# Kernel optimization log

Measured on AMD Instinct MI355X. Metric: run time of the kernel, lower is better.

## Reference

```python
import jax, jax.numpy as jnp
import numpy as np

USER_NUM = 50000
ITEM_NUM = 50000
N = USER_NUM + ITEM_NUM
VT_DIM = 512
CAT_NUM = 1000
CAT_DIM = 32
HIDDEN = 128
OUT = 64
E = 2_000_000
BAG = 5


def setup_inputs() -> dict:
    key = jax.random.key(0)
    ks = jax.random.split(key, 12)
    inp = {
        "vt_feature": jax.random.normal(ks[0], (ITEM_NUM, VT_DIM), jnp.float32),
        "cat_indices": jax.random.randint(ks[1], (ITEM_NUM * BAG,), 0, CAT_NUM),
        "cat_offsets": jnp.arange(ITEM_NUM) * BAG,
        "edge_index": jax.random.randint(ks[2], (2, E), 0, N),
        # learned parameters
        "cat_table": jax.random.normal(ks[3], (CAT_NUM, CAT_DIM), jnp.float32) * 0.1,
        "fuse_w": jax.random.normal(ks[4], (HIDDEN, VT_DIM + CAT_DIM), jnp.float32) * (1.0 / np.sqrt(VT_DIM + CAT_DIM)),
        "user": jax.random.normal(ks[5], (USER_NUM, HIDDEN), jnp.float32) * 0.1,
        "w1_l": jax.random.normal(ks[6], (HIDDEN, HIDDEN), jnp.float32) * (1.0 / np.sqrt(HIDDEN)),
        "b1": jnp.zeros((HIDDEN,), jnp.float32),
        "w1_r": jax.random.normal(ks[7], (HIDDEN, HIDDEN), jnp.float32) * (1.0 / np.sqrt(HIDDEN)),
        "w2_l": jax.random.normal(ks[8], (OUT, HIDDEN), jnp.float32) * (1.0 / np.sqrt(HIDDEN)),
        "b2": jnp.zeros((OUT,), jnp.float32),
        "w2_r": jax.random.normal(ks[9], (OUT, HIDDEN), jnp.float32) * (1.0 / np.sqrt(HIDDEN)),
    }
    return inp


def _embedding_bag_mean(table, indices, offsets, num_bags):
    # EmbeddingBag(mode='mean') with offsets: segment-mean of table lookups.
    pos = jnp.arange(indices.shape[0])
    seg = jnp.searchsorted(offsets, pos, side="right") - 1  # bag id per index
    sums = jax.ops.segment_sum(table[indices], seg, num_segments=num_bags)
    cnt = jax.ops.segment_sum(jnp.ones_like(pos, jnp.float32), seg, num_segments=num_bags)
    return sums / jnp.maximum(cnt, 1.0)[:, None]


def _sage_conv(x, edge_index, w_l, b_l, w_r):
    # PyG SAGEConv (aggr='mean'): lin_l(mean_{j->i} x_j) + lin_r(x_i)
    src, dst = edge_index[0], edge_index[1]
    agg = jax.ops.segment_sum(x[src], dst, num_segments=N)
    deg = jax.ops.segment_sum(jnp.ones((src.shape[0],), x.dtype), dst, num_segments=N)
    agg = agg / jnp.maximum(deg, 1.0)[:, None]
    return agg @ w_l.T + b_l + x @ w_r.T


def reference(vt_feature, cat_indices, cat_offsets, edge_index, cat_table,
              fuse_w, user, w1_l, b1, w1_r, w2_l, b2, w2_r):
    cat_emb = _embedding_bag_mean(cat_table, cat_indices, cat_offsets, ITEM_NUM)
    item_feat = jnp.concatenate([vt_feature, cat_emb], axis=1) @ fuse_w.T
    x0 = jnp.concatenate([user, item_feat], axis=0)  # [N, hidden]
    x1 = jax.nn.leaky_relu(_sage_conv(x0, edge_index, w1_l, b1, w1_r), negative_slope=0.01)
    # dropout is identity in eval mode
    x2 = _sage_conv(x1, edge_index, w2_l, b2, w2_r)
    return x2
```

## Files before the change

### kernel.cpp

```cpp
#include <hip/hip_runtime.h>

#define USER_N   50000
#define ITEM_N   50000
#define NNODE    100000
#define VT_DIM   512
#define CAT_DIM  32
#define HIDDEN   128
#define OUTD     64
#define PADCAP   64

typedef __attribute__((ext_vector_type(8))) short short8;
typedef __attribute__((ext_vector_type(4))) float f32x4;

__device__ __forceinline__ float bf2f(unsigned short u) {
    return __uint_as_float(((unsigned int)u) << 16);
}
__device__ __forceinline__ unsigned short f2bf(float f) {
    unsigned int u = __float_as_uint(f);
    unsigned int r = u + 0x7fffu + ((u >> 16) & 1u);
    return (unsigned short)(r >> 16);
}

__global__ __launch_bounds__(256) void k_catemb(const float* __restrict__ cat_table,
                                                const int* __restrict__ cat_idx,
                                                const int* __restrict__ cat_off,
                                                unsigned short* __restrict__ catemb,
                                                int item_num, int total_idx) {
    int gid = blockIdx.x * 256 + threadIdx.x;
    int item = gid >> 5;
    int d = gid & 31;
    if (item >= item_num) return;
    int s = cat_off[item];
    int e = (item + 1 < item_num) ? cat_off[item + 1] : total_idx;
    float acc = 0.f;
    for (int j = s; j < e; ++j) {
        int idx = cat_idx[j];
        acc += cat_table[idx * CAT_DIM + d];
    }
    int cnt = e - s;
    float inv = 1.f / (float)(cnt > 0 ? cnt : 1);
    catemb[(size_t)item * CAT_DIM + d] = f2bf(acc * inv);
}

__global__ __launch_bounds__(256) void k_copy_user(const float* __restrict__ user,
                                                   unsigned short* __restrict__ x0, int n4) {
    int gid = blockIdx.x * 256 + threadIdx.x;
    if (gid >= n4) return;
    float4 v = ((const float4*)user)[gid];
    ushort4 o;
    o.x = f2bf(v.x); o.y = f2bf(v.y); o.z = f2bf(v.z); o.w = f2bf(v.w);
    ((ushort4*)x0)[gid] = o;
}

#define ASTR 40

__global__ __launch_bounds__(256, 2) void k_fuse_mfma(const float* __restrict__ vt,
                                                      const unsigned short* __restrict__ catemb,
                                                      const float* __restrict__ fw,
                                                      unsigned short* __restrict__ x0) {
    __shared__ __align__(16) unsigned short Al[256 * ASTR];
    __shared__ __align__(16) unsigned short Bl[128 * ASTR];
    int tid = threadIdx.x;
    int wave = tid >> 6, lane = tid & 63, quad = lane >> 4, l16 = lane & 15;
    int br0 = blockIdx.x * 256;
    int arow = br0 + tid;

    f32x4 acc[4][8];
#pragma unroll
    for (int m = 0; m < 4; m++)
#pragma unroll
        for (int n = 0; n < 8; n++) acc[m][n] = (f32x4){0.f, 0.f, 0.f, 0.f};

    for (int kb = 0; kb < 17; ++kb) {
        if (kb < 16) {
            if (arow < ITEM_N) {
                const float* src = vt + (size_t)arow * VT_DIM + kb * 32;
#pragma unroll
                for (int i = 0; i < 8; i++) {
                    float4 v = ((const float4*)src)[i];
                    ushort4 o;
                    o.x = f2bf(v.x); o.y = f2bf(v.y); o.z = f2bf(v.z); o.w = f2bf(v.w);
                    *(ushort4*)&Al[tid * ASTR + i * 4] = o;
                }
            } else {
                ushort4 z = {0, 0, 0, 0};
#pragma unroll
                for (int i = 0; i < 8; i++) *(ushort4*)&Al[tid * ASTR + i * 4] = z;
            }
        } else {
            if (arow < ITEM_N) {
                const uint4* src = (const uint4*)(catemb + (size_t)arow * CAT_DIM);
                *(uint4*)&Al[tid * ASTR]      = src[0];
                *(uint4*)&Al[tid * ASTR + 8]  = src[1];
                *(uint4*)&Al[tid * ASTR + 16] = src[2];
                *(uint4*)&Al[tid * ASTR + 24] = src[3];
            } else {
                uint4 z = {0, 0, 0, 0};
                *(uint4*)&Al[tid * ASTR]      = z;
                *(uint4*)&Al[tid * ASTR + 8]  = z;
                *(uint4*)&Al[tid * ASTR + 16] = z;
                *(uint4*)&Al[tid * ASTR + 24] = z;
            }
        }
        {
            int n = tid & 127, kh = tid >> 7;
            const float* src = fw + (size_t)n * (VT_DIM + CAT_DIM) + kb * 32 + kh * 16;
#pragma unroll
            for (int i = 0; i < 4; i++) {
                float4 v = ((const float4*)src)[i];
                ushort4 o;
                o.x = f2bf(v.x); o.y = f2bf(v.y); o.z = f2bf(v.z); o.w = f2bf(v.w);
                *(ushort4*)&Bl[n * ASTR + kh * 16 + i * 4] = o;
            }
        }
        __syncthreads();
        short8 av[4];
#pragma unroll
        for (int m = 0; m < 4; m++)
            av[m] = *(const short8*)&Al[(wave * 64 + m * 16 + l16) * ASTR + quad * 8];
#pragma unroll
        for (int nf = 0; nf < 8; nf++) {
            short8 bv = *(const short8*)&Bl[(nf * 16 + l16) * ASTR + quad * 8];
#pragma unroll
            for (int m = 0; m < 4; m++)
                acc[m][nf] = __builtin_amdgcn_mfma_f32_16x16x32_bf16(av[m], bv, acc[m][nf], 0, 0, 0);
        }
        __syncthreads();
    }
    int rbase = br0 + wave * 64;
#pragma unroll
    for (int m = 0; m < 4; m++) {
#pragma unroll
        for (int r = 0; r < 4; r++) {
            int row = rbase + m * 16 + quad * 4 + r;
            if (row < ITEM_N) {
#pragma unroll
                for (int nf = 0; nf < 8; nf++) {
                    int col = nf * 16 + l16;
                    x0[(size_t)(USER_N + row) * HIDDEN + col] = f2bf(acc[m][nf][r]);
                }
            }
        }
    }
}

__global__ __launch_bounds__(256, 2) void k_l1_mfma(const unsigned short* __restrict__ agg1,
                                                    const unsigned short* __restrict__ x0,
                                                    const float* __restrict__ w1l,
                                                    const float* __restrict__ w1r,
                                                    const float* __restrict__ b1,
                                                    unsigned short* __restrict__ x1) {
    __shared__ __align__(16) unsigned short Al[256 * ASTR];
    __shared__ __align__(16) unsigned short Bl[128 * ASTR];
    int tid = threadIdx.x;
    int wave = tid >> 6, lane = tid & 63, quad = lane >> 4, l16 = lane & 15;
    int br0 = blockIdx.x * 256;
    int arow = br0 + tid;

    f32x4 acc[4][8];
#pragma unroll
    for (int m = 0; m < 4; m++)
#pragma unroll
        for (int n = 0; n < 8; n++) acc[m][n] = (f32x4){0.f, 0.f, 0.f, 0.f};

    for (int kb = 0; kb < 8; ++kb) {
        const unsigned short* abase = (kb < 4) ? agg1 : x0;
        int kc = (kb & 3) * 32;
        if (arow < NNODE) {
            const uint4* src = (const uint4*)(abase + (size_t)arow * HIDDEN + kc);
            *(uint4*)&Al[tid * ASTR]      = src[0];
            *(uint4*)&Al[tid * ASTR + 8]  = src[1];
            *(uint4*)&Al[tid * ASTR + 16] = src[2];
            *(uint4*)&Al[tid * ASTR + 24] = src[3];
        } else {
            uint4 z = {0, 0, 0, 0};
            *(uint4*)&Al[tid * ASTR]      = z;
            *(uint4*)&Al[tid * ASTR + 8]  = z;
            *(uint4*)&Al[tid * ASTR + 16] = z;
            *(uint4*)&Al[tid * ASTR + 24] = z;
        }
        {
            int n = tid & 127, kh = tid >> 7;
            const float* src = ((kb < 4) ? w1l : w1r) + (size_t)n * HIDDEN + kc + kh * 16;
#pragma unroll
            for (int i = 0; i < 4; i++) {
                float4 v = ((const float4*)src)[i];
                ushort4 o;
                o.x = f2bf(v.x); o.y = f2bf(v.y); o.z = f2bf(v.z); o.w = f2bf(v.w);
                *(ushort4*)&Bl[n * ASTR + kh * 16 + i * 4] = o;
            }
        }
        __syncthreads();
        short8 av[4];
#pragma unroll
        for (int m = 0; m < 4; m++)
            av[m] = *(const short8*)&Al[(wave * 64 + m * 16 + l16) * ASTR + quad * 8];
#pragma unroll
        for (int nf = 0; nf < 8; nf++) {
            short8 bv = *(const short8*)&Bl[(nf * 16 + l16) * ASTR + quad * 8];
#pragma unroll
            for (int m = 0; m < 4; m++)
                acc[m][nf] = __builtin_amdgcn_mfma_f32_16x16x32_bf16(av[m], bv, acc[m][nf], 0, 0, 0);
        }
        __syncthreads();
    }
    float bias[8];
#pragma unroll
    for (int nf = 0; nf < 8; nf++) bias[nf] = b1[nf * 16 + l16];
    int rbase = br0 + wave * 64;
#pragma unroll
    for (int m = 0; m < 4; m++) {
#pragma unroll
        for (int r = 0; r < 4; r++) {
            int row = rbase + m * 16 + quad * 4 + r;
            if (row < NNODE) {
#pragma unroll
                for (int nf = 0; nf < 8; nf++) {
                    int col = nf * 16 + l16;
                    float v = acc[m][nf][r] + bias[nf];
                    v = (v >= 0.f) ? v : 0.01f * v;
                    x1[(size_t)row * HIDDEN + col] = f2bf(v);
                }
            }
        }
    }
}

__global__ __launch_bounds__(256, 2) void k_l2_mfma(const unsigned short* __restrict__ x1,
                                                    const float* __restrict__ w2l,
                                                    const float* __restrict__ w2r,
                                                    const float* __restrict__ b2,
                                                    unsigned short* __restrict__ y1,
                                                    float* __restrict__ outw) {
    __shared__ __align__(16) unsigned short Al[256 * ASTR];
    __shared__ __align__(16) unsigned short Bl[128 * ASTR];
    int tid = threadIdx.x;
    int wave = tid >> 6, lane = tid & 63, quad = lane >> 4, l16 = lane & 15;
    int br0 = blockIdx.x * 256;
    int arow = br0 + tid;

    f32x4 acc[4][8];
#pragma unroll
    for (int m = 0; m < 4; m++)
#pragma unroll
        for (int n = 0; n < 8; n++) acc[m][n] = (f32x4){0.f, 0.f, 0.f, 0.f};

    for (int kb = 0; kb < 4; ++kb) {
        int kc = kb * 32;
        if (arow < NNODE) {
            const uint4* src = (const uint4*)(x1 + (size_t)arow * HIDDEN + kc);
            *(uint4*)&Al[tid * ASTR]      = src[0];
            *(uint4*)&Al[tid * ASTR + 8]  = src[1];
            *(uint4*)&Al[tid * ASTR + 16] = src[2];
            *(uint4*)&Al[tid * ASTR + 24] = src[3];
        } else {
            uint4 z = {0, 0, 0, 0};
            *(uint4*)&Al[tid * ASTR]      = z;
            *(uint4*)&Al[tid * ASTR + 8]  = z;
            *(uint4*)&Al[tid * ASTR + 16] = z;
            *(uint4*)&Al[tid * ASTR + 24] = z;
        }
        {
            int n = tid & 127, kh = tid >> 7;
            const float* wsrc = (n < 64) ? (w2l + (size_t)n * HIDDEN)
                                         : (w2r + (size_t)(n - 64) * HIDDEN);
            const float* src = wsrc + kc + kh * 16;
#pragma unroll
            for (int i = 0; i < 4; i++) {
                float4 v = ((const float4*)src)[i];
                ushort4 o;
                o.x = f2bf(v.x); o.y = f2bf(v.y); o.z = f2bf(v.z); o.w = f2bf(v.w);
                *(ushort4*)&Bl[n * ASTR + kh * 16 + i * 4] = o;
            }
        }
        __syncthreads();
        short8 av[4];
#pragma unroll
        for (int m = 0; m < 4; m++)
            av[m] = *(const short8*)&Al[(wave * 64 + m * 16 + l16) * ASTR + quad * 8];
#pragma unroll
        for (int nf = 0; nf < 8; nf++) {
            short8 bv = *(const short8*)&Bl[(nf * 16 + l16) * ASTR + quad * 8];
#pragma unroll
            for (int m = 0; m < 4; m++)
                acc[m][nf] = __builtin_amdgcn_mfma_f32_16x16x32_bf16(av[m], bv, acc[m][nf], 0, 0, 0);
        }
        __syncthreads();
    }
    float bias2[4];
#pragma unroll
    for (int nf = 0; nf < 4; nf++) bias2[nf] = b2[nf * 16 + l16];
    int rbase = br0 + wave * 64;
#pragma unroll
    for (int m = 0; m < 4; m++) {
#pragma unroll
        for (int r = 0; r < 4; r++) {
            int row = rbase + m * 16 + quad * 4 + r;
            if (row < NNODE) {
#pragma unroll
                for (int nf = 0; nf < 4; nf++) {
                    int col = nf * 16 + l16;
                    y1[(size_t)row * OUTD + col] = f2bf(acc[m][nf][r]);
                }
#pragma unroll
                for (int nf = 4; nf < 8; nf++) {
                    int col = (nf - 4) * 16 + l16;
                    outw[(size_t)row * OUTD + col] = acc[m][nf][r] + bias2[nf - 4];
                }
            }
        }
    }
}

__global__ __launch_bounds__(256) void k_deg(const int* __restrict__ dst, int ne4, int ne, int* __restrict__ deg) {
    int t = blockIdx.x * 256 + threadIdx.x;
    int base = t * 4;
    if (t < ne4) {
        int4 d4 = *(const int4*)&dst[base];
        atomicAdd(&deg[d4.x], 1);
        atomicAdd(&deg[d4.y], 1);
        atomicAdd(&deg[d4.z], 1);
        atomicAdd(&deg[d4.w], 1);
    } else {
        for (int e = base; e < ne; ++e) atomicAdd(&deg[dst[e]], 1);
    }
}

__global__ __launch_bounds__(256) void k_scanA(const int* __restrict__ deg, int n, int* __restrict__ bsum) {
    __shared__ int sd[256];
    int i = blockIdx.x * 256 + threadIdx.x;
    sd[threadIdx.x] = (i < n) ? deg[i] : 0;
    __syncthreads();
    for (int o = 128; o > 0; o >>= 1) {
        if (threadIdx.x < o) sd[threadIdx.x] += sd[threadIdx.x + o];
        __syncthreads();
    }
    if (threadIdx.x == 0) bsum[blockIdx.x] = sd[0];
}

__global__ __launch_bounds__(512) void k_scanB(const int* __restrict__ bsum, int nb, int* __restrict__ boff) {
    __shared__ int sd[512];
    int t = threadIdx.x;
    int v = (t < nb) ? bsum[t] : 0;
    sd[t] = v;
    __syncthreads();
    for (int o = 1; o < 512; o <<= 1) {
        int x = 0;
        if (t >= o) x = sd[t - o];
        __syncthreads();
        sd[t] += x;
        __syncthreads();
    }
    if (t < nb) boff[t] = sd[t] - v;
}

__global__ __launch_bounds__(256) void k_scanC(const int* __restrict__ deg, int n,
                                               const int* __restrict__ boff,
                                               int* __restrict__ offs, int* __restrict__ cursor, int ne) {
    __shared__ int sd[256];
    int i = blockIdx.x * 256 + threadIdx.x;
    int v = (i < n) ? deg[i] : 0;
    sd[threadIdx.x] = v;
    __syncthreads();
    for (int o = 1; o < 256; o <<= 1) {
        int x = 0;
        if (threadIdx.x >= o) x = sd[threadIdx.x - o];
        __syncthreads();
        sd[threadIdx.x] += x;
        __syncthreads();
    }
    if (i < n) {
        int ex = boff[blockIdx.x] + sd[threadIdx.x] - v;
        offs[i] = ex;
        cursor[i] = ex;
    }
    if (i == 0) offs[n] = ne;
}

__global__ __launch_bounds__(256) void k_scatter(const int* __restrict__ src, const int* __restrict__ dst,
                                                 int ne4, int ne, int* __restrict__ cursor, int* __restrict__ csr) {
    int t = blockIdx.x * 256 + threadIdx.x;
    int base = t * 4;
    if (t < ne4) {
        int4 d4 = *(const int4*)&dst[base];
        int4 s4 = *(const int4*)&src[base];
        int p0 = atomicAdd(&cursor[d4.x], 1);
        int p1 = atomicAdd(&cursor[d4.y], 1);
        int p2 = atomicAdd(&cursor[d4.z], 1);
        int p3 = atomicAdd(&cursor[d4.w], 1);
        csr[p0] = s4.x;
        csr[p1] = s4.y;
        csr[p2] = s4.z;
        csr[p3] = s4.w;
    } else {
        for (int e = base; e < ne; ++e) {
            int slot = atomicAdd(&cursor[dst[e]], 1);
            csr[slot] = src[e];
        }
    }
}

__global__ __launch_bounds__(256) void k_scatter_pad(const int* __restrict__ src, const int* __restrict__ dst,
                                                     int ne4, int ne, int* __restrict__ cursor,
                                                     int* __restrict__ csrp) {
    int t = blockIdx.x * 256 + threadIdx.x;
    int base = t * 4;
    if (t < ne4) {
        int4 d4 = *(const int4*)&dst[base];
        int4 s4 = *(const int4*)&src[base];
        int p0 = atomicAdd(&cursor[d4.x], 1);
        int p1 = atomicAdd(&cursor[d4.y], 1);
        int p2 = atomicAdd(&cursor[d4.z], 1);
        int p3 = atomicAdd(&cursor[d4.w], 1);
        if (p0 < PADCAP) csrp[d4.x * PADCAP + p0] = s4.x;
        if (p1 < PADCAP) csrp[d4.y * PADCAP + p1] = s4.y;
        if (p2 < PADCAP) csrp[d4.z * PADCAP + p2] = s4.z;
        if (p3 < PADCAP) csrp[d4.w * PADCAP + p3] = s4.w;
    } else {
        for (int e = base; e < ne; ++e) {
            int d = dst[e];
            int slot = atomicAdd(&cursor[d], 1);
            if (slot < PADCAP) csrp[d * PADCAP + slot] = src[e];
        }
    }
}

__global__ __launch_bounds__(256) void k_agg1(const unsigned short* __restrict__ x0,
                                              const int* __restrict__ offs,
                                              const int* __restrict__ cnts,
                                              int pad,
                                              const int* __restrict__ csr,
                                              unsigned short* __restrict__ agg1) {
    int wid = (blockIdx.x << 2) + (threadIdx.x >> 6);
    if (wid >= NNODE) return;
    int lane = threadIdx.x & 63;
    int half = lane >> 5;
    int l32 = lane & 31;
    int s, e, d;
    if (pad) {
        s = wid << 6;
        int c = cnts[wid];
        d = c;
        e = s + (c < PADCAP ? c : PADCAP);
    } else {
        s = offs[wid];
        e = offs[wid + 1];
        d = e - s;
    }
    float a0 = 0.f, a1 = 0.f, a2 = 0.f, a3 = 0.f;
    int j = s;
    for (; j + 16 <= e; j += 16) {
        int sn[8];
#pragma unroll
        for (int u = 0; u < 8; u++) sn[u] = csr[j + 2 * u + half];
        ushort4 v[8];
#pragma unroll
        for (int u = 0; u < 8; u++) v[u] = *(const ushort4*)&x0[(size_t)sn[u] * HIDDEN + l32 * 4];
#pragma unroll
        for (int u = 0; u < 8; u++) {
            a0 += bf2f(v[u].x);
            a1 += bf2f(v[u].y);
            a2 += bf2f(v[u].z);
            a3 += bf2f(v[u].w);
        }
    }
    for (; j + 8 <= e; j += 8) {
        int sn0 = csr[j     + half];
        int sn1 = csr[j + 2 + half];
        int sn2 = csr[j + 4 + half];
        int sn3 = csr[j + 6 + half];
        ushort4 v0 = *(const ushort4*)&x0[(size_t)sn0 * HIDDEN + l32 * 4];
        ushort4 v1 = *(const ushort4*)&x0[(size_t)sn1 * HIDDEN + l32 * 4];
        ushort4 v2 = *(const ushort4*)&x0[(size_t)sn2 * HIDDEN + l32 * 4];
        ushort4 v3 = *(const ushort4*)&x0[(size_t)sn3 * HIDDEN + l32 * 4];
        a0 += bf2f(v0.x) + bf2f(v1.x) + bf2f(v2.x) + bf2f(v3.x);
        a1 += bf2f(v0.y) + bf2f(v1.y) + bf2f(v2.y) + bf2f(v3.y);
        a2 += bf2f(v0.z) + bf2f(v1.z) + bf2f(v2.z) + bf2f(v3.z);
        a3 += bf2f(v0.w) + bf2f(v1.w) + bf2f(v2.w) + bf2f(v3.w);
    }
    for (; j < e; j += 2) {
        int myj = j + half;
        bool ok = (myj < e);
        int sn = ok ? csr[myj] : csr[j];
        float w = ok ? 1.f : 0.f;
        ushort4 v = *(const ushort4*)&x0[(size_t)sn * HIDDEN + l32 * 4];
        a0 += w * bf2f(v.x);
        a1 += w * bf2f(v.y);
        a2 += w * bf2f(v.z);
        a3 += w * bf2f(v.w);
    }
    a0 += __shfl_xor(a0, 32, 64);
    a1 += __shfl_xor(a1, 32, 64);
    a2 += __shfl_xor(a2, 32, 64);
    a3 += __shfl_xor(a3, 32, 64);
    float inv = 1.f / (float)(d > 0 ? d : 1);
    if (half == 0) {
        ushort4 o;
        o.x = f2bf(a0 * inv);
        o.y = f2bf(a1 * inv);
        o.z = f2bf(a2 * inv);
        o.w = f2bf(a3 * inv);
        *(ushort4*)&agg1[(size_t)wid * HIDDEN + l32 * 4] = o;
    }
}

__global__ __launch_bounds__(256) void k_agg2_out(const unsigned short* __restrict__ y1,
                                                  const int* __restrict__ offs,
                                                  const int* __restrict__ cnts,
                                                  int pad,
                                                  const int* __restrict__ csr,
                                                  float* __restrict__ out) {
    int wid = (blockIdx.x << 2) + (threadIdx.x >> 6);
    if (wid >= NNODE) return;
    int lane = threadIdx.x & 63;
    int quad = lane >> 4;
    int l16 = lane & 15;
    int s, e, d;
    if (pad) {
        s = wid << 6;
        int c = cnts[wid];
        d = c;
        e = s + (c < PADCAP ? c : PADCAP);
    } else {
        s = offs[wid];
        e = offs[wid + 1];
        d = e - s;
    }
    float a0 = 0.f, a1 = 0.f, a2 = 0.f, a3 = 0.f;
    int j = s;
    for (; j + 16 <= e; j += 16) {
        int sn0 = csr[j      + quad];
        int sn1 = csr[j + 4  + quad];
        int sn2 = csr[j + 8  + quad];
        int sn3 = csr[j + 12 + quad];
        ushort4 v0 = *(const ushort4*)&y1[(size_t)sn0 * OUTD + l16 * 4];
        ushort4 v1 = *(const ushort4*)&y1[(size_t)sn1 * OUTD + l16 * 4];
        ushort4 v2 = *(const ushort4*)&y1[(size_t)sn2 * OUTD + l16 * 4];
        ushort4 v3 = *(const ushort4*)&y1[(size_t)sn3 * OUTD + l16 * 4];
        a0 += bf2f(v0.x) + bf2f(v1.x) + bf2f(v2.x) + bf2f(v3.x);
        a1 += bf2f(v0.y) + bf2f(v1.y) + bf2f(v2.y) + bf2f(v3.y);
        a2 += bf2f(v0.z) + bf2f(v1.z) + bf2f(v2.z) + bf2f(v3.z);
        a3 += bf2f(v0.w) + bf2f(v1.w) + bf2f(v2.w) + bf2f(v3.w);
    }
    for (; j < e; j += 4) {
        int myj = j + quad;
        bool ok = (myj < e);
        int sn = ok ? csr[myj] : csr[j];
        float w = ok ? 1.f : 0.f;
        ushort4 v = *(const ushort4*)&y1[(size_t)sn * OUTD + l16 * 4];
        a0 += w * bf2f(v.x);
        a1 += w * bf2f(v.y);
        a2 += w * bf2f(v.z);
        a3 += w * bf2f(v.w);
    }
    a0 += __shfl_xor(a0, 16, 64);
    a1 += __shfl_xor(a1, 16, 64);
    a2 += __shfl_xor(a2, 16, 64);
    a3 += __shfl_xor(a3, 16, 64);
    a0 += __shfl_xor(a0, 32, 64);
    a1 += __shfl_xor(a1, 32, 64);
    a2 += __shfl_xor(a2, 32, 64);
    a3 += __shfl_xor(a3, 32, 64);
    float inv = 1.f / (float)(d > 0 ? d : 1);
    if (quad == 0) {
        float4* op = (float4*)&out[(size_t)wid * OUTD + l16 * 4];
        float4 prev = *op;
        float4 o;
        o.x = a0 * inv + prev.x;
        o.y = a1 * inv + prev.y;
        o.z = a2 * inv + prev.z;
        o.w = a3 * inv + prev.w;
        *op = o;
    }
}

extern "C" void kernel_launch(void* const* d_in, const int* in_sizes, int n_in,
                              void* d_out, int out_size, void* d_ws, size_t ws_size,
                              hipStream_t stream) {
    const float* vt      = (const float*)d_in[0];
    const int*   cat_idx = (const int*)d_in[1];
    const int*   cat_off = (const int*)d_in[2];
    const int*   ei      = (const int*)d_in[3];
    const float* cat_tab = (const float*)d_in[4];
    const float* fuse_w  = (const float*)d_in[5];
    const float* user    = (const float*)d_in[6];
    const float* w1l     = (const float*)d_in[7];
    const float* b1      = (const float*)d_in[8];
    const float* w1r     = (const float*)d_in[9];
    const float* w2l     = (const float*)d_in[10];
    const float* b2      = (const float*)d_in[11];
    const float* w2r     = (const float*)d_in[12];
    float* out = (float*)d_out;

    const int ne = in_sizes[3] / 2;
    const int ne4 = ne / 4;
    const int total_idx = in_sizes[1];
    const int* esrc = ei;
    const int* edst = ei + ne;

    const size_t SZ_X0  = (size_t)NNODE * HIDDEN * 2;
    const size_t SZ_PAD = (size_t)NNODE * PADCAP * 4;
    const size_t SZ_CSR = (size_t)ne * 4;
    const size_t SZ_INT = (size_t)NNODE * 4;

    size_t need_pad = SZ_X0 * 3 + SZ_PAD + SZ_INT + 8192;
    size_t need_csr = SZ_X0 * 3 + SZ_CSR + SZ_INT * 3 + 4 * 4096 + 4096;

    char* p = (char*)d_ws;
    auto alloc = [&](size_t bytes) {
        char* q = p;
        p += (bytes + 255) & ~(size_t)255;
        return q;
    };

    const int nscan = (NNODE + 255) / 256;
    const int sc_blocks = (ne4 + 255) / 256;

    if (ws_size >= need_pad) {
        unsigned short* x0   = (unsigned short*)alloc(SZ_X0);
        unsigned short* aggY = (unsigned short*)alloc(SZ_X0);
        unsigned short* x1   = (unsigned short*)alloc(SZ_X0);
        int*            csrp = (int*)alloc(SZ_PAD);
        int*          cursor = (int*)alloc(SZ_INT);
        unsigned short* catemb = (unsigned short*)csrp;

        k_catemb<<<(ITEM_N * 32 + 255) / 256, 256, 0, stream>>>(cat_tab, cat_idx, cat_off, catemb, ITEM_N, total_idx);
        k_copy_user<<<(USER_N * HIDDEN / 4 + 255) / 256, 256, 0, stream>>>(user, x0, USER_N * HIDDEN / 4);
        k_fuse_mfma<<<(ITEM_N + 255) / 256, 256, 0, stream>>>(vt, catemb, fuse_w, x0);

        hipMemsetAsync(cursor, 0, SZ_INT, stream);
        k_scatter_pad<<<sc_blocks, 256, 0, stream>>>(esrc, edst, ne4, ne, cursor, csrp);

        k_agg1<<<(NNODE + 3) / 4, 256, 0, stream>>>(x0, cursor, cursor, 1, csrp, aggY);
        k_l1_mfma<<<(NNODE + 255) / 256, 256, 0, stream>>>(aggY, x0, w1l, w1r, b1, x1);
        k_l2_mfma<<<(NNODE + 255) / 256, 256, 0, stream>>>(x1, w2l, w2r, b2, aggY, out);
        k_agg2_out<<<(NNODE + 3) / 4, 256, 0, stream>>>(aggY, cursor, cursor, 1, csrp, out);
    } else if (ws_size >= need_csr) {
        unsigned short* x0   = (unsigned short*)alloc(SZ_X0);
        unsigned short* aggY = (unsigned short*)alloc(SZ_X0);
        unsigned short* x1   = (unsigned short*)alloc(SZ_X0);
        char*           R4   = (char*)alloc(SZ_CSR);
        int* deg    = (int*)alloc(SZ_INT);
        int* offs   = (int*)alloc(SZ_INT + 256);
        int* cursor = (int*)alloc(SZ_INT);
        int* bsum   = (int*)alloc(512 * 4);
        int* boff   = (int*)alloc(512 * 4);
        unsigned short* catemb = (unsigned short*)R4;
        int*            csr    = (int*)R4;

        k_catemb<<<(ITEM_N * 32 + 255) / 256, 256, 0, stream>>>(cat_tab, cat_idx, cat_off, catemb, ITEM_N, total_idx);
        k_copy_user<<<(USER_N * HIDDEN / 4 + 255) / 256, 256, 0, stream>>>(user, x0, USER_N * HIDDEN / 4);
        k_fuse_mfma<<<(ITEM_N + 255) / 256, 256, 0, stream>>>(vt, catemb, fuse_w, x0);

        hipMemsetAsync(deg, 0, SZ_INT, stream);
        k_deg<<<sc_blocks, 256, 0, stream>>>(edst, ne4, ne, deg);
        k_scanA<<<nscan, 256, 0, stream>>>(deg, NNODE, bsum);
        k_scanB<<<1, 512, 0, stream>>>(bsum, nscan, boff);
        k_scanC<<<nscan, 256, 0, stream>>>(deg, NNODE, boff, offs, cursor, ne);
        k_scatter<<<sc_blocks, 256, 0, stream>>>(esrc, edst, ne4, ne, cursor, csr);

        k_agg1<<<(NNODE + 3) / 4, 256, 0, stream>>>(x0, offs, offs, 0, csr, aggY);
        k_l1_mfma<<<(NNODE + 255) / 256, 256, 0, stream>>>(aggY, x0, w1l, w1r, b1, x1);
        k_l2_mfma<<<(NNODE + 255) / 256, 256, 0, stream>>>(x1, w2l, w2r, b2, aggY, out);
        k_agg2_out<<<(NNODE + 3) / 4, 256, 0, stream>>>(aggY, offs, offs, 0, csr, out);
    } else {
        hipMemsetAsync(d_out, 0, (size_t)out_size * 4, stream);
    }
}
```

Before: 582.0 us.

## Bucket edges by destination range before padded CSR scatter for locality

Measured after the change: 536.8 us. 7.8% less time.

```diff
diff --git a/kernel.cpp b/kernel.cpp
--- a/kernel.cpp
+++ b/kernel.cpp
@@ -8,6 +8,11 @@
 #define HIDDEN   128
 #define OUTD     64
 #define PADCAP   64
+
+#define BINC    8192
+#define NBKT    98
+#define BSHIFT  10
+#define SLICES  8
 
 typedef __attribute__((ext_vector_type(8))) short short8;
 typedef __attribute__((ext_vector_type(4))) float f32x4;
@@ -425,6 +430,87 @@
     }
 }
 
+__global__ __launch_bounds__(256) void k_hist(const int* __restrict__ dst, int ne,
+                                              int nblk, int* __restrict__ hist) {
+    __shared__ int lh[NBKT];
+    int b = blockIdx.x;
+    for (int i = threadIdx.x; i < NBKT; i += 256) lh[i] = 0;
+    __syncthreads();
+    int s = b * BINC;
+    int e = (s + BINC < ne) ? (s + BINC) : ne;
+    for (int j = s + threadIdx.x; j < e; j += 256) {
+        atomicAdd(&lh[dst[j] >> BSHIFT], 1);
+    }
+    __syncthreads();
+    for (int i = threadIdx.x; i < NBKT; i += 256) hist[i * nblk + b] = lh[i];
+}
+
+__global__ __launch_bounds__(1024) void k_scan1(int* __restrict__ hist, int tot) {
+    __shared__ int ls[1024];
+    int t = threadIdx.x;
+    int K = (tot + 1023) >> 10;
+    int base = t * K;
+    int end = base + K;
+    if (end > tot) end = tot;
+    int s = 0;
+    for (int i = base; i < end; ++i) s += hist[i];
+    ls[t] = s;
+    __syncthreads();
+    for (int o = 1; o < 1024; o <<= 1) {
+        int v = (t >= o) ? ls[t - o] : 0;
+        __syncthreads();
+        ls[t] += v;
+        __syncthreads();
+    }
+    int run = ls[t] - s;
+    for (int i = base; i < end; ++i) {
+        int tmp = hist[i];
+        hist[i] = run;
+        run += tmp;
+    }
+}
+
+__global__ __launch_bounds__(256) void k_binscatter(const int* __restrict__ src,
+                                                    const int* __restrict__ dst,
+                                                    int ne, int nblk,
+                                                    const int* __restrict__ hist,
+                                                    int2* __restrict__ ebin) {
+    __shared__ int lc[NBKT];
+    int b = blockIdx.x;
+    for (int i = threadIdx.x; i < NBKT; i += 256) lc[i] = hist[i * nblk + b];
+    __syncthreads();
+    int s = b * BINC;
+    int e = (s + BINC < ne) ? (s + BINC) : ne;
+    for (int j = s + threadIdx.x; j < e; j += 256) {
+        int d = dst[j];
+        int p = atomicAdd(&lc[d >> BSHIFT], 1);
+        ebin[p] = make_int2(src[j], d);
+    }
+}
+
+__global__ __launch_bounds__(256) void k_scatter_bkt(const int2* __restrict__ ebin,
+                                                     const int* __restrict__ hist,
+                                                     int nblk, int ne,
+                                                     int* __restrict__ cursor,
+                                                     int* __restrict__ csrp) {
+    int xcd = blockIdx.x & 7;
+    int w = blockIdx.x >> 3;
+    int i = w / SLICES, sl = w - i * SLICES;
+    int b = xcd + (i << 3);
+    if (b >= NBKT) return;
+    int s0 = hist[b * nblk];
+    int e0 = (b + 1 < NBKT) ? hist[(b + 1) * nblk] : ne;
+    int len = e0 - s0;
+    int per = (len + SLICES - 1) / SLICES;
+    int s = s0 + sl * per;
+    int e = (s + per < e0) ? (s + per) : e0;
+    for (int j = s + threadIdx.x; j < e; j += 256) {
+        int2 p = ebin[j];
+        int slot = atomicAdd(&cursor[p.y], 1);
+        if (slot < PADCAP) csrp[p.y * PADCAP + slot] = p.x;
+    }
+}
+
 __global__ __launch_bounds__(256) void k_agg1(const unsigned short* __restrict__ x0,
                                               const int* __restrict__ offs,
                                               const int* __restrict__ cnts,
@@ -629,7 +715,20 @@
         k_fuse_mfma<<<(ITEM_N + 255) / 256, 256, 0, stream>>>(vt, catemb, fuse_w, x0);
 
         hipMemsetAsync(cursor, 0, SZ_INT, stream);
-        k_scatter_pad<<<sc_blocks, 256, 0, stream>>>(esrc, edst, ne4, ne, cursor, csrp);
+
+        const int nblk = (ne + BINC - 1) / BINC;
+        bool fast_bin = ((size_t)ne * sizeof(int2) <= SZ_X0) &&
+                        ((size_t)NBKT * nblk * sizeof(int) <= SZ_X0);
+        if (fast_bin) {
+            int*  hist = (int*)aggY;
+            int2* ebin = (int2*)x1;
+            k_hist<<<nblk, 256, 0, stream>>>(edst, ne, nblk, hist);
+            k_scan1<<<1, 1024, 0, stream>>>(hist, NBKT * nblk);
+            k_binscatter<<<nblk, 256, 0, stream>>>(esrc, edst, ne, nblk, hist, ebin);
+            k_scatter_bkt<<<8 * 13 * SLICES, 256, 0, stream>>>(ebin, hist, nblk, ne, cursor, csrp);
+        } else {
+            k_scatter_pad<<<sc_blocks, 256, 0, stream>>>(esrc, edst, ne4, ne, cursor, csrp);
+        }
 
         k_agg1<<<(NNODE + 3) / 4, 256, 0, stream>>>(x0, cursor, cursor, 1, csrp, aggY);
         k_l1_mfma<<<(NNODE + 255) / 256, 256, 0, stream>>>(aggY, x0, w1l, w1r, b1, x1);
```
